# Kernel tuning notes

Measured on AMD Instinct MI355X. Metric: run time of the kernel, lower is better.

Reference implementation:

```python
import jax, jax.numpy as jnp
import numpy as np
from jax import lax

B, C, H, W, NH = 16, 512, 32, 32, 8
HC = C // NH  # head channels = 64


def setup_inputs() -> dict:
    key = jax.random.key(0)
    ks = jax.random.split(key, 8)
    rn = lambda i, shape, scale: jax.random.normal(ks[i], shape, jnp.float32) * scale
    return dict(
        image=jax.random.normal(ks[0], (B, C, H, W), jnp.float32),
        watermark=jax.random.normal(ks[1], (B, C, H, W), jnp.float32),
        img_ln_w=jnp.ones((C, H, W), jnp.float32),
        img_ln_b=jnp.zeros((C, H, W), jnp.float32),
        wm_ln_w=jnp.ones((C, H, W), jnp.float32),
        wm_ln_b=jnp.zeros((C, H, W), jnp.float32),
        img_pw_w=rn(2, (3 * C, C), 0.02),
        img_pw_b=jnp.zeros((3 * C,), jnp.float32),
        img_dw_w=rn(3, (3 * C, 3, 3, 3), 0.1),
        img_dw_b=jnp.zeros((3 * C,), jnp.float32),
        wm_pw_w=rn(4, (3 * C, C), 0.02),
        wm_pw_b=jnp.zeros((3 * C,), jnp.float32),
        wm_dw_w=rn(5, (3 * C, 3, 3, 3), 0.1),
        wm_dw_b=jnp.zeros((3 * C,), jnp.float32),
        proj=rn(6, (2 * C, C), 0.02),
    )


def _layernorm(x, w, b, eps=1e-5):
    # LayerNorm over [C,H,W] per sample, elementwise affine of shape [C,H,W]
    mu = jnp.mean(x, axis=(1, 2, 3), keepdims=True)
    var = jnp.mean((x - mu) ** 2, axis=(1, 2, 3), keepdims=True)
    return (x - mu) * lax.rsqrt(var + eps) * w + b


def _dconv_proj(x, pw_w, pw_b, dw_w, dw_b):
    # pointwise 1x1 conv C -> 3C
    x = jnp.einsum('bchw,oc->bohw', x, pw_w) + pw_b[None, :, None, None]
    # depthwise 3x3 conv on 3C channels with groups=C (3 channels per group)
    x = lax.conv_general_dilated(
        x, dw_w, window_strides=(1, 1), padding='SAME',
        dimension_numbers=('NCHW', 'OIHW', 'NCHW'), feature_group_count=C)
    x = x + dw_b[None, :, None, None]
    return jnp.split(x, 3, axis=1)  # Q, K, V each [B,C,H,W]


def reference(image, watermark, img_ln_w, img_ln_b, wm_ln_w, wm_ln_b,
              img_pw_w, img_pw_b, img_dw_w, img_dw_b,
              wm_pw_w, wm_pw_b, wm_dw_w, wm_dw_b, proj):
    img = _layernorm(image, img_ln_w, img_ln_b)
    wm = _layernorm(watermark, wm_ln_w, wm_ln_b)
    Qi, Ki, Vi = _dconv_proj(img, img_pw_w, img_pw_b, img_dw_w, img_dw_b)
    Qw, Kw, Vw = _dconv_proj(wm, wm_pw_w, wm_pw_b, wm_dw_w, wm_dw_b)
    r = lambda t: t.reshape(B, NH, HC, H * W)
    Qi, Ki, Vi, Qw, Kw, Vw = map(r, (Qi, Ki, Vi, Qw, Kw, Vw))
    # NOTE: original code calls F.normalize but discards the result -> no-op.
    Kc = jnp.concatenate([Ki, Kw], axis=2)  # [B,NH,2*HC,HW]
    Vc = jnp.concatenate([Vi, Vw], axis=2)  # [B,NH,2*HC,HW]
    # scores: K_concat @ Q^T over the HW axis -> [B,NH,2*HC,HC], softmax over HC
    Ai = jax.nn.softmax(jnp.einsum('bnkp,bnqp->bnkq', Kc, Qi), axis=-1)
    Aw = jax.nn.softmax(jnp.einsum('bnkp,bnqp->bnkq', Kc, Qw), axis=-1)
    # A^T @ V_concat -> [B,NH,HC,HW]
    img_attn = jnp.einsum('bnkq,bnkp->bnqp', Ai, Vc)
    wm_attn = jnp.einsum('bnkq,bnkp->bnqp', Aw, Vc)
    attn = jnp.concatenate([img_attn, wm_attn], axis=2).reshape(B, 2 * C, H, W)
    # final channel-mixing projection: [B,H,W,2C] @ [2C,C] -> [B,C,H,W]
    return jnp.einsum('bdhw,dc->bchw', attn, proj)
```

## Files before the change

### kernel.cpp

```cpp
#include <hip/hip_runtime.h>
#include <hip/hip_bf16.h>
#include <stdint.h>

#define Bn  16
#define Cch 512
#define C3  1536
#define HWp 1024

typedef __attribute__((ext_vector_type(8))) short bf16x8;
typedef __attribute__((ext_vector_type(4))) float f32x4;

#define DEV static __device__ __forceinline__

DEV float bflo(unsigned u) { return __builtin_bit_cast(float, u << 16); }
DEV float bfhi(unsigned u) { return __builtin_bit_cast(float, u & 0xffff0000u); }
DEV unsigned short f2bf(float f) {
  __hip_bfloat16 h = __float2bfloat16(f);
  return __builtin_bit_cast(unsigned short, h);
}

DEV void async16(__hip_bfloat16* lds, const __hip_bfloat16* g) {
  __builtin_amdgcn_global_load_lds(
      (const __attribute__((address_space(1))) unsigned*)g,
      (__attribute__((address_space(3))) unsigned*)lds, 16, 0, 0);
}

__global__ __launch_bounds__(256) void k_prep_ln(
    const float* __restrict__ img_pw_w, const float* __restrict__ wm_pw_w,
    const float* __restrict__ proj,
    const float* __restrict__ image, const float* __restrict__ watermark,
    __hip_bfloat16* __restrict__ Wpw, __hip_bfloat16* __restrict__ projT,
    float* __restrict__ part)
{
  __shared__ float ls[4], lss[4];
  int blkid = blockIdx.x;
  if (blkid < 8192) {
    int i = blkid * 256 + threadIdx.x;
    const int NW = C3 * Cch;
    if (i < NW)          Wpw[i] = __float2bfloat16(img_pw_w[i]);
    else if (i < 2 * NW) Wpw[i] = __float2bfloat16(wm_pw_w[i - NW]);
    else {
      int j = i - 2 * NW;
      int c = j >> 10, d = j & 1023;
      projT[(size_t)c * 1024 + d] = __float2bfloat16(proj[(size_t)d * 512 + c]);
    }
    return;
  }
  int blk = blkid - 8192;
  int chunk = blk & 63, b = (blk >> 6) & 15, t = blk >> 10;
  const float* x = (t ? watermark : image) + (size_t)b * Cch * HWp + chunk * 8192;
  const float4* xv = (const float4*)x;
  float s = 0.f, ss = 0.f;
#pragma unroll
  for (int i = 0; i < 8; i++) {
    float4 v = xv[threadIdx.x + i * 256];
    s  += v.x + v.y + v.z + v.w;
    ss += v.x * v.x + v.y * v.y + v.z * v.z + v.w * v.w;
  }
#pragma unroll
  for (int off = 32; off; off >>= 1) { s += __shfl_down(s, off); ss += __shfl_down(ss, off); }
  int wv = threadIdx.x >> 6;
  if ((threadIdx.x & 63) == 0) { ls[wv] = s; lss[wv] = ss; }
  __syncthreads();
  if (threadIdx.x == 0) {
    part[blk * 2]     = ls[0] + ls[1] + ls[2] + ls[3];
    part[blk * 2 + 1] = lss[0] + lss[1] + lss[2] + lss[3];
  }
}

__global__ void k_ln_final(const float* __restrict__ part, float* __restrict__ stats)
{
  int i = threadIdx.x;
  if (i < 32) {
    float S = 0.f, SS = 0.f;
    for (int c2 = 0; c2 < 64; c2++) { S += part[(i * 64 + c2) * 2]; SS += part[(i * 64 + c2) * 2 + 1]; }
    const float inv = 1.f / (float)(Cch * HWp);
    float mu  = S * inv;
    float var = SS * inv - mu * mu;
    stats[i]      = mu;
    stats[32 + i] = rsqrtf(var + 1e-5f);
  }
}

__global__ __launch_bounds__(256) void k_norm_t(
    const float* __restrict__ image, const float* __restrict__ watermark,
    const float* __restrict__ img_w, const float* __restrict__ img_b,
    const float* __restrict__ wm_w,  const float* __restrict__ wm_b,
    const float* __restrict__ stats, __hip_bfloat16* __restrict__ xnT)
{
  int blk = blockIdx.x;
  int ct = blk & 15, pt = (blk >> 4) & 15, b = (blk >> 8) & 15, t = blk >> 12;
  int c0 = ct * 32, p0 = pt * 64;
  const float* x   = (t ? watermark : image) + (size_t)b * Cch * HWp;
  const float* wgt = t ? wm_w : img_w;
  const float* bia = t ? wm_b : img_b;
  float mu = stats[t * 16 + b], rstd = stats[32 + t * 16 + b];
  __shared__ float tile[32 * 66];
  int tid = threadIdx.x;
  {
    int c = tid >> 3, s = tid & 7;
    const float* xr = x   + (size_t)(c0 + c) * HWp + p0;
    const float* wr = wgt + (size_t)(c0 + c) * HWp + p0;
    const float* br = bia + (size_t)(c0 + c) * HWp + p0;
#pragma unroll
    for (int j = 0; j < 2; j++) {
      int f = s + j * 8;
      float4 xv = *(const float4*)&xr[f * 4];
      float4 wv = *(const float4*)&wr[f * 4];
      float4 bv = *(const float4*)&br[f * 4];
      float n0 = (xv.x - mu) * rstd * wv.x + bv.x;
      float n1 = (xv.y - mu) * rstd * wv.y + bv.y;
      float n2 = (xv.z - mu) * rstd * wv.z + bv.z;
      float n3 = (xv.w - mu) * rstd * wv.w + bv.w;
      *(float2*)&tile[c * 66 + f * 4]     = make_float2(n0, n1);
      *(float2*)&tile[c * 66 + f * 4 + 2] = make_float2(n2, n3);
    }
  }
  __syncthreads();
  {
    int p = tid >> 2, cq = tid & 3;
    union { unsigned short us[8]; uint4 v4; } pk;
#pragma unroll
    for (int j = 0; j < 8; j++) pk.us[j] = f2bf(tile[(cq * 8 + j) * 66 + p]);
    __hip_bfloat16* dst = xnT + ((size_t)(t * 16 + b)) * HWp * Cch
                        + (size_t)(p0 + p) * Cch + c0 + cq * 8;
    *(uint4*)dst = pk.v4;
  }
}

template<int MI, int Kdim, int Ncols, bool OBF, bool HB>
DEV void gemm_core(const __hip_bfloat16* __restrict__ A,
                   const __hip_bfloat16* __restrict__ Bt,
                   const float* __restrict__ bias, void* __restrict__ Cout)
{
  constexpr int MT = MI * 32;
  __shared__ __hip_bfloat16 As[MT * 64];
  __shared__ __hip_bfloat16 Bs[128 * 64];
  const int tid = threadIdx.x, lane = tid & 63, wv = tid >> 6;
  const int lr = lane & 15, lq = lane >> 4;
  const int wm = (wv >> 1) * (MI * 16), wn = (wv & 1) * 64;
  const int m0 = blockIdx.y * MT, n0 = blockIdx.x * 128;
  f32x4 acc[MI][4] = {};
  const int srow = tid >> 3, sslot = tid & 7;
  const int sseg = (sslot ^ (srow & 7)) * 8;
  for (int k0 = 0; k0 < Kdim; k0 += 64) {
#pragma unroll
    for (int c = 0; c < MI; c++) {
      int row = srow + c * 32;
      async16(&As[row * 64 + sslot * 8], &A[(size_t)(m0 + row) * Kdim + k0 + sseg]);
    }
#pragma unroll
    for (int c = 0; c < 4; c++) {
      int row = srow + c * 32;
      async16(&Bs[row * 64 + sslot * 8], &Bt[(size_t)(n0 + row) * Kdim + k0 + sseg]);
    }
    __syncthreads();
#pragma unroll
    for (int ks = 0; ks < 2; ks++) {
      bf16x8 af[MI], bfr[4];
#pragma unroll
      for (int mi = 0; mi < MI; mi++) {
        int r = wm + mi * 16 + lr;
        af[mi]  = *(const bf16x8*)&As[r * 64 + (((ks * 4 + lq) ^ (lr & 7)) * 8)];
      }
#pragma unroll
      for (int ni = 0; ni < 4; ni++) {
        int r = wn + ni * 16 + lr;
        bfr[ni] = *(const bf16x8*)&Bs[r * 64 + (((ks * 4 + lq) ^ (lr & 7)) * 8)];
      }
#pragma unroll
      for (int mi = 0; mi < MI; mi++)
#pragma unroll
        for (int ni = 0; ni < 4; ni++)
          acc[mi][ni] = __builtin_amdgcn_mfma_f32_16x16x32_bf16(af[mi], bfr[ni], acc[mi][ni], 0, 0, 0);
    }
    __syncthreads();
  }
#pragma unroll
  for (int mi = 0; mi < MI; mi++) {
    int mrow = m0 + wm + mi * 16 + lq * 4;
#pragma unroll
    for (int ni = 0; ni < 4; ni++) {
      int ncol = n0 + wn + ni * 16 + lr;
#pragma unroll
      for (int r = 0; r < 4; r++) {
        float y = acc[mi][ni][r];
        int row = mrow + r;
        if (HB) y += bias[row];
        if (OBF) ((__hip_bfloat16*)Cout)[(size_t)row * Ncols + ncol] = __float2bfloat16(y);
        else     ((float*)Cout)[(size_t)row * Ncols + ncol] = y;
      }
    }
  }
}

__global__ __launch_bounds__(256) void k_pw_gemm(
    const __hip_bfloat16* __restrict__ Wpw, const __hip_bfloat16* __restrict__ xnT,
    const float* __restrict__ img_pw_b, const float* __restrict__ wm_pw_b,
    __hip_bfloat16* __restrict__ Y)
{
  int bz = blockIdx.z, t = bz >> 4;
  gemm_core<4, 512, 1024, true, true>(
      Wpw + (size_t)t * C3 * Cch,
      xnT + (size_t)bz * HWp * Cch,
      t ? wm_pw_b : img_pw_b,
      Y + (size_t)bz * C3 * HWp);
}

__global__ __launch_bounds__(256) void k_proj_gemm(
    const __hip_bfloat16* __restrict__ projT, const __hip_bfloat16* __restrict__ attnT,
    float* __restrict__ out)
{
  int b = blockIdx.z;
  gemm_core<2, 1024, 1024, false, false>(
      projT, attnT + (size_t)b * HWp * 1024, nullptr, out + (size_t)b * Cch * HWp);
}

__global__ __launch_bounds__(256) void k_dw(
    const __hip_bfloat16* __restrict__ Y,
    const float* __restrict__ img_dw_w, const float* __restrict__ img_dw_b,
    const float* __restrict__ wm_dw_w,  const float* __restrict__ wm_dw_b,
    __hip_bfloat16* __restrict__ QKV)
{
  int idx = blockIdx.x * 256 + threadIdx.x;
  int w0 = (idx & 3) * 8;
  int h  = (idx >> 2) & 31;
  int g  = __builtin_amdgcn_readfirstlane((idx >> 7) & 511);
  int tb = __builtin_amdgcn_readfirstlane(idx >> 16);
  int t  = tb >> 4;
  const float* dww = (t ? wm_dw_w : img_dw_w) + g * 81;
  const float* dwb = (t ? wm_dw_b : img_dw_b) + g * 3;
  const __hip_bfloat16* base = Y + ((size_t)tb * C3 + g * 3) * HWp;
  float acc[3][8];
#pragma unroll
  for (int o = 0; o < 3; o++) {
    float bv = dwb[o];
#pragma unroll
    for (int w = 0; w < 8; w++) acc[o][w] = bv;
  }
  const bool mlo = (w0 == 0), mhi = (w0 == 24);
#pragma unroll
  for (int i = 0; i < 3; i++) {
#pragma unroll
    for (int kh = 0; kh < 3; kh++) {
      int hh = h + kh - 1;
      if ((unsigned)hh > 31u) continue;
      const unsigned* up = (const unsigned*)(base + i * HWp + hh * 32 + (w0 - 2));
      float v[12];
#pragma unroll
      for (int d2 = 0; d2 < 6; d2++) { unsigned u = up[d2]; v[d2*2] = bflo(u); v[d2*2+1] = bfhi(u); }
      if (mlo) { v[0] = 0.f; v[1] = 0.f; }
      if (mhi) { v[10] = 0.f; v[11] = 0.f; }
#pragma unroll
      for (int o = 0; o < 3; o++) {
        float wk0 = dww[o*27 + i*9 + kh*3 + 0];
        float wk1 = dww[o*27 + i*9 + kh*3 + 1];
        float wk2 = dww[o*27 + i*9 + kh*3 + 2];
#pragma unroll
        for (int w = 0; w < 8; w++)
          acc[o][w] += v[w + 1] * wk0 + v[w + 2] * wk1 + v[w + 3] * wk2;
      }
    }
  }
#pragma unroll
  for (int o = 0; o < 3; o++) {
    union { unsigned short us[8]; uint4 v4; } pk;
#pragma unroll
    for (int w = 0; w < 8; w++) pk.us[w] = f2bf(acc[o][w]);
    *(uint4*)(QKV + ((size_t)tb * C3 + g * 3 + o) * HWp + h * 32 + w0) = pk.v4;
  }
}

__global__ __launch_bounds__(256) void k_attn_scores(
    const __hip_bfloat16* __restrict__ QKV, __hip_bfloat16* __restrict__ ATg)
{
  int blk = blockIdx.x, kh = blk & 1, m = (blk >> 1) & 1, bn = blk >> 2;
  int b = bn >> 3, nh = bn & 7;
  int tid = threadIdx.x, lane = tid & 63, wv = tid >> 6;
  int lr = lane & 15, lq = lane >> 4;
  const __hip_bfloat16* kb =
      QKV + (((size_t)(kh * 16 + b)) * C3 + 512 + nh * 64 + (wv * 16 + lr)) * HWp + lq * 8;
  const __hip_bfloat16* qbase[4];
#pragma unroll
  for (int qt = 0; qt < 4; qt++)
    qbase[qt] = QKV + (((size_t)(m * 16 + b)) * C3 + nh * 64 + qt * 16 + lr) * HWp + lq * 8;

  f32x4 acc[4] = {};
  for (int p0 = 0; p0 < HWp; p0 += 32) {
    bf16x8 bk = *(const bf16x8*)(kb + p0);
#pragma unroll
    for (int qt = 0; qt < 4; qt++) {
      bf16x8 aq = *(const bf16x8*)(qbase[qt] + p0);
      acc[qt] = __builtin_amdgcn_mfma_f32_16x16x32_bf16(aq, bk, acc[qt], 0, 0, 0);
    }
  }
  __shared__ float S[64][65];
  __shared__ float redmax[4][64];
  __shared__ float redsum[4][64];
  __shared__ __hip_bfloat16 Ash[64][72];
#pragma unroll
  for (int qt = 0; qt < 4; qt++)
#pragma unroll
    for (int r = 0; r < 4; r++)
      S[qt * 16 + lq * 4 + r][wv * 16 + lr] = acc[qt][r];
  __syncthreads();
  int k = tid & 63, sub = tid >> 6;
  float vals[16], mx = -1e30f;
#pragma unroll
  for (int j = 0; j < 16; j++) { vals[j] = S[sub * 16 + j][k]; mx = fmaxf(mx, vals[j]); }
  redmax[sub][k] = mx;
  __syncthreads();
  float M = fmaxf(fmaxf(redmax[0][k], redmax[1][k]), fmaxf(redmax[2][k], redmax[3][k]));
  float ssum = 0.f;
#pragma unroll
  for (int j = 0; j < 16; j++) { vals[j] = __expf(vals[j] - M); ssum += vals[j]; }
  redsum[sub][k] = ssum;
  __syncthreads();
  float inv = 1.f / (redsum[0][k] + redsum[1][k] + redsum[2][k] + redsum[3][k]);
#pragma unroll
  for (int j = 0; j < 16; j++) Ash[sub * 16 + j][k] = __float2bfloat16(vals[j] * inv);
  __syncthreads();
  __hip_bfloat16* outp = ATg + ((size_t)(bn * 2 + m)) * 64 * 128 + kh * 64;
#pragma unroll
  for (int s = 0; s < 2; s++) {
    int id = tid + s * 256, row = id >> 3, seg = (id & 7) * 8;
    *(uint4*)&outp[(size_t)row * 128 + seg] = *(const uint4*)&Ash[row][seg];
  }
}

__global__ __launch_bounds__(256) void k_attn_out(
    const __hip_bfloat16* __restrict__ QKV, const __hip_bfloat16* __restrict__ ATg,
    __hip_bfloat16* __restrict__ attnT)
{
  int blk = blockIdx.x, pc = blk & 3, bn = blk >> 2, b = bn >> 3, nh = bn & 7;
  int tid = threadIdx.x, lane = tid & 63, wv = tid >> 6;
  int lr = lane & 15, lq = lane >> 4;
  __shared__ __hip_bfloat16 ATs[2][64][136];
  __shared__ __hip_bfloat16 VTs[64][136];
#pragma unroll
  for (int m = 0; m < 2; m++) {
    const __hip_bfloat16* src = ATg + ((size_t)(bn * 2 + m)) * 64 * 128;
#pragma unroll
    for (int s = 0; s < 4; s++) {
      int id = tid + s * 256, row = id >> 4, seg = (id & 15) * 8;
      *(uint4*)&ATs[m][row][seg] = *(const uint4*)&src[row * 128 + seg];
    }
  }
  const int vk0 = (tid >> 3) * 4, vps = (tid & 7) * 8;
  for (int ps = 0; ps < 4; ps++) {
    int p0 = pc * 256 + ps * 64;
    __syncthreads();
    union { uint4 v4; unsigned short us[8]; } ld[4];
#pragma unroll
    for (int j = 0; j < 4; j++) {
      int kk = vk0 + j, tk = kk >> 6, hc = kk & 63;
      ld[j].v4 = *(const uint4*)(QKV +
          (((size_t)(tk * 16 + b)) * C3 + 1024 + nh * 64 + hc) * HWp + p0 + vps);
    }
#pragma unroll
    for (int e = 0; e < 8; e++) {
      uint2 w;
      w.x = (unsigned)ld[0].us[e] | ((unsigned)ld[1].us[e] << 16);
      w.y = (unsigned)ld[2].us[e] | ((unsigned)ld[3].us[e] << 16);
      *(uint2*)&VTs[vps + e][vk0] = w;
    }
    __syncthreads();
#pragma unroll
    for (int m = 0; m < 2; m++) {
      f32x4 oacc[4] = {};
#pragma unroll
      for (int ks = 0; ks < 4; ks++) {
        bf16x8 bv = *(const bf16x8*)&VTs[wv * 16 + lr][ks * 32 + lq * 8];
#pragma unroll
        for (int qt = 0; qt < 4; qt++) {
          bf16x8 av = *(const bf16x8*)&ATs[m][qt * 16 + lr][ks * 32 + lq * 8];
          oacc[qt] = __builtin_amdgcn_mfma_f32_16x16x32_bf16(av, bv, oacc[qt], 0, 0, 0);
        }
      }
#pragma unroll
      for (int qt = 0; qt < 4; qt++) {
        int q = qt * 16 + lq * 4;
        int d = nh * 128 + m * 64 + q;
        int p = p0 + wv * 16 + lr;
        union { unsigned short us[4]; uint2 v2; } pk;
#pragma unroll
        for (int r = 0; r < 4; r++) pk.us[r] = f2bf(oacc[qt][r]);
        *(uint2*)&attnT[((size_t)b * HWp + p) * 1024 + d] = pk.v2;
      }
    }
  }
}

extern "C" void kernel_launch(void* const* d_in, const int* in_sizes, int n_in,
                              void* d_out, int out_size, void* d_ws, size_t ws_size,
                              hipStream_t stream)
{
  (void)in_sizes; (void)n_in; (void)out_size; (void)ws_size;
  const float* image     = (const float*)d_in[0];
  const float* watermark = (const float*)d_in[1];
  const float* img_ln_w  = (const float*)d_in[2];
  const float* img_ln_b  = (const float*)d_in[3];
  const float* wm_ln_w   = (const float*)d_in[4];
  const float* wm_ln_b   = (const float*)d_in[5];
  const float* img_pw_w  = (const float*)d_in[6];
  const float* img_pw_b  = (const float*)d_in[7];
  const float* img_dw_w  = (const float*)d_in[8];
  const float* img_dw_b  = (const float*)d_in[9];
  const float* wm_pw_w   = (const float*)d_in[10];
  const float* wm_pw_b   = (const float*)d_in[11];
  const float* wm_dw_w   = (const float*)d_in[12];
  const float* wm_dw_b   = (const float*)d_in[13];
  const float* proj      = (const float*)d_in[14];

  char* ws = (char*)d_ws;
  __hip_bfloat16* Wpw    = (__hip_bfloat16*)(ws + 0);
  __hip_bfloat16* projT  = (__hip_bfloat16*)(ws + 3145728);
  float*          lnpart = (float*)(ws + 4194304);
  float*          stats  = (float*)(ws + 4210688);
  __hip_bfloat16* xnT    = (__hip_bfloat16*)(ws + 5242880);
  __hip_bfloat16* attnT  = xnT;
  __hip_bfloat16* Y      = (__hip_bfloat16*)(ws + 41943040);
  __hip_bfloat16* ATg    = Y;
  __hip_bfloat16* QKV    = (__hip_bfloat16*)(ws + 142606336);

  k_prep_ln<<<10240, 256, 0, stream>>>(img_pw_w, wm_pw_w, proj, image, watermark,
                                       Wpw, projT, lnpart);
  k_ln_final<<<1, 64, 0, stream>>>(lnpart, stats);
  k_norm_t<<<8192, 256, 0, stream>>>(image, watermark, img_ln_w, img_ln_b,
                                     wm_ln_w, wm_ln_b, stats, xnT);
  dim3 gpw(8, 12, 32);
  k_pw_gemm<<<gpw, 256, 0, stream>>>(Wpw, xnT, img_pw_b, wm_pw_b, Y);
  k_dw<<<8192, 256, 0, stream>>>(Y, img_dw_w, img_dw_b, wm_dw_w, wm_dw_b, QKV);
  k_attn_scores<<<512, 256, 0, stream>>>(QKV, ATg);
  k_attn_out<<<512, 256, 0, stream>>>(QKV, ATg, attnT);
  dim3 gpj(8, 8, 16);
  k_proj_gemm<<<gpj, 256, 0, stream>>>(projT, attnT, (float*)d_out);
}
```

Before: 374.5 us.

## Use 256x256 double-buffered pointwise GEMM tile and larger proj GEMM M-tile

Replaces the generic pointwise GEMM with a dedicated 512-thread kernel computing 256x256 output tiles. It double-buffers A/B tiles in swizzled LDS via async global-to-LDS loads and interleaves the next stage's loads between two MFMA k-halves, with wave priority raised during compute. The projection GEMM switches to a larger M-tile template (MI=4) with half the grid rows. The goal is more data reuse per LDS load and better overlap of memory and matrix math, at the cost of 128KB LDS and many more accumulator registers per thread, which lowers occupancy.

```diff
diff --git a/kernel.cpp b/kernel.cpp
--- a/kernel.cpp
+++ b/kernel.cpp
@@ -194,17 +194,96 @@
   }
 }
 
-__global__ __launch_bounds__(256) void k_pw_gemm(
+__global__ __launch_bounds__(512) void k_pw_gemm256(
     const __hip_bfloat16* __restrict__ Wpw, const __hip_bfloat16* __restrict__ xnT,
     const float* __restrict__ img_pw_b, const float* __restrict__ wm_pw_b,
     __hip_bfloat16* __restrict__ Y)
 {
-  int bz = blockIdx.z, t = bz >> 4;
-  gemm_core<4, 512, 1024, true, true>(
-      Wpw + (size_t)t * C3 * Cch,
-      xnT + (size_t)bz * HWp * Cch,
-      t ? wm_pw_b : img_pw_b,
-      Y + (size_t)bz * C3 * HWp);
+  constexpr int K = 512, NT = K / 64;
+  __shared__ __hip_bfloat16 lds[2][2][256 * 64];
+  const int bz = blockIdx.z, t = bz >> 4;
+  const __hip_bfloat16* Ag = Wpw + (size_t)t * C3 * Cch;
+  const __hip_bfloat16* Bg = xnT + (size_t)bz * HWp * Cch;
+  const float* bias = t ? wm_pw_b : img_pw_b;
+  __hip_bfloat16* Co = Y + (size_t)bz * C3 * HWp;
+  const int m0 = blockIdx.y * 256, n0 = blockIdx.x * 256;
+  const int tid = threadIdx.x, lane = tid & 63, wv = tid >> 6;
+  const int lr = lane & 15, lq = lane >> 4;
+  const int wm = (wv >> 2) * 128, wn = (wv & 3) * 64;
+  const int srow = tid >> 3, sslot = tid & 7;
+  const int sseg = (sslot ^ (srow & 7)) * 8;
+  f32x4 acc[8][4] = {};
+
+  auto stage = [&](int kt) {
+    const int p = kt & 1;
+    const __hip_bfloat16* Ak = Ag + (size_t)(m0 + srow) * K + kt * 64 + sseg;
+    const __hip_bfloat16* Bk = Bg + (size_t)(n0 + srow) * K + kt * 64 + sseg;
+    __hip_bfloat16* La = &lds[p][0][srow * 64 + sslot * 8];
+    __hip_bfloat16* Lb = &lds[p][1][srow * 64 + sslot * 8];
+#pragma unroll
+    for (int c = 0; c < 4; c++) {
+      async16(La + c * 64 * 64, Ak + (size_t)c * 64 * K);
+      async16(Lb + c * 64 * 64, Bk + (size_t)c * 64 * K);
+    }
+  };
+
+  stage(0);
+  stage(1);
+  for (int kt = 0; kt < NT; ++kt) {
+    if (kt < NT - 1) asm volatile("s_waitcnt vmcnt(8)" ::: "memory");
+    else             asm volatile("s_waitcnt vmcnt(0)" ::: "memory");
+    __builtin_amdgcn_s_barrier();
+    __builtin_amdgcn_sched_barrier(0);
+    const int p = kt & 1;
+    const __hip_bfloat16* As = lds[p][0];
+    const __hip_bfloat16* Bs = lds[p][1];
+    bf16x8 af[2][8], bfr[2][4];
+#pragma unroll
+    for (int ks = 0; ks < 2; ks++) {
+#pragma unroll
+      for (int mi = 0; mi < 8; mi++) {
+        int r = wm + mi * 16 + lr;
+        af[ks][mi] = *(const bf16x8*)&As[r * 64 + (((ks * 4 + lq) ^ (lr & 7)) * 8)];
+      }
+#pragma unroll
+      for (int ni = 0; ni < 4; ni++) {
+        int r = wn + ni * 16 + lr;
+        bfr[ks][ni] = *(const bf16x8*)&Bs[r * 64 + (((ks * 4 + lq) ^ (lr & 7)) * 8)];
+      }
+    }
+    __builtin_amdgcn_s_setprio(1);
+#pragma unroll
+    for (int mi = 0; mi < 8; mi++)
+#pragma unroll
+      for (int ni = 0; ni < 4; ni++)
+        acc[mi][ni] = __builtin_amdgcn_mfma_f32_16x16x32_bf16(af[0][mi], bfr[0][ni], acc[mi][ni], 0, 0, 0);
+    __builtin_amdgcn_s_setprio(0);
+    asm volatile("s_waitcnt lgkmcnt(0)" ::: "memory");
+    __builtin_amdgcn_sched_barrier(0);
+    __builtin_amdgcn_s_barrier();
+    __builtin_amdgcn_sched_barrier(0);
+    if (kt + 2 < NT) stage(kt + 2);
+    __builtin_amdgcn_s_setprio(1);
+#pragma unroll
+    for (int mi = 0; mi < 8; mi++)
+#pragma unroll
+      for (int ni = 0; ni < 4; ni++)
+        acc[mi][ni] = __builtin_amdgcn_mfma_f32_16x16x32_bf16(af[1][mi], bfr[1][ni], acc[mi][ni], 0, 0, 0);
+    __builtin_amdgcn_s_setprio(0);
+  }
+#pragma unroll
+  for (int mi = 0; mi < 8; mi++) {
+    int mrow = m0 + wm + mi * 16 + lq * 4;
+#pragma unroll
+    for (int ni = 0; ni < 4; ni++) {
+      int ncol = n0 + wn + ni * 16 + lr;
+#pragma unroll
+      for (int r = 0; r < 4; r++) {
+        float y = acc[mi][ni][r] + bias[mrow + r];
+        Co[(size_t)(mrow + r) * HWp + ncol] = __float2bfloat16(y);
+      }
+    }
+  }
 }
 
 __global__ __launch_bounds__(256) void k_proj_gemm(
@@ -212,7 +291,7 @@
     float* __restrict__ out)
 {
   int b = blockIdx.z;
-  gemm_core<2, 1024, 1024, false, false>(
+  gemm_core<4, 1024, 1024, false, false>(
       projT, attnT + (size_t)b * HWp * 1024, nullptr, out + (size_t)b * Cch * HWp);
 }
 
@@ -428,11 +507,11 @@
   k_ln_final<<<1, 64, 0, stream>>>(lnpart, stats);
   k_norm_t<<<8192, 256, 0, stream>>>(image, watermark, img_ln_w, img_ln_b,
                                      wm_ln_w, wm_ln_b, stats, xnT);
-  dim3 gpw(8, 12, 32);
-  k_pw_gemm<<<gpw, 256, 0, stream>>>(Wpw, xnT, img_pw_b, wm_pw_b, Y);
+  dim3 gpw(4, 6, 32);
+  k_pw_gemm256<<<gpw, 512, 0, stream>>>(Wpw, xnT, img_pw_b, wm_pw_b, Y);
   k_dw<<<8192, 256, 0, stream>>>(Y, img_dw_w, img_dw_b, wm_dw_w, wm_dw_b, QKV);
   k_attn_scores<<<512, 256, 0, stream>>>(QKV, ATg);
   k_attn_out<<<512, 256, 0, stream>>>(QKV, ATg, attnT);
-  dim3 gpj(8, 8, 16);
+  dim3 gpj(8, 4, 16);
   k_proj_gemm<<<gpj, 256, 0, stream>>>(projT, attnT, (float*)d_out);
 }
```

After: 381.9 us. Within noise of the previous version (+2.0%).
